# Performance work log

Measured on AMD Instinct MI355X. Metric: run time of the kernel, lower is better.

The kernel has to match this reference:

```python
import jax, jax.numpy as jnp
import numpy as np

B, T, H, L = 64, 2048, 256, 16


def setup_inputs() -> dict:
    key = jax.random.key(0)
    ks = jax.random.split(key, 6)
    x = jax.random.normal(ks[0], (B, T, H), dtype=jnp.float32)
    tags = jax.random.randint(ks[1], (B, T), 0, L).astype(jnp.int32)
    mask = jnp.ones((B, T), dtype=bool)  # torchcrf requires mask[:,0] all on
    W = jax.random.normal(ks[2], (L, H), dtype=jnp.float32) * (1.0 / np.sqrt(H))
    b = jnp.zeros((L,), dtype=jnp.float32)
    # torchcrf initializes transitions ~ U(-0.1, 0.1)
    start_transitions = jax.random.uniform(ks[3], (L,), minval=-0.1, maxval=0.1)
    end_transitions = jax.random.uniform(ks[4], (L,), minval=-0.1, maxval=0.1)
    transitions = jax.random.uniform(ks[5], (L, L), minval=-0.1, maxval=0.1)
    return {"x": x, "W": W, "b": b,
            "start_transitions": start_transitions,
            "end_transitions": end_transitions,
            "transitions": transitions,
            "tags": tags, "mask": mask}


def reference(x, W, b, start_transitions, end_transitions, transitions, tags, mask):
    # Emitter: Linear(hidden_dim -> num_labels)
    emissions = jnp.einsum('bth,lh->btl', x, W) + b  # [B,T,L]
    maskf = mask.astype(emissions.dtype)             # [B,T]

    # ---- numerator: score of the gold tag path (vectorized, no scan) ----
    emit_gold = jnp.take_along_axis(emissions, tags[..., None].astype(jnp.int32), axis=2)[..., 0]  # [B,T]
    first_tags = tags[:, 0]
    score = start_transitions[first_tags] + emit_gold[:, 0]
    trans_gold = transitions[tags[:, :-1], tags[:, 1:]]  # [B,T-1]
    score = score + jnp.sum((trans_gold + emit_gold[:, 1:]) * maskf[:, 1:], axis=1)
    seq_ends = jnp.sum(mask.astype(jnp.int32), axis=1) - 1  # index of last valid step
    last_tags = jnp.take_along_axis(tags, seq_ends[:, None], axis=1)[:, 0]
    score = score + end_transitions[last_tags]

    # ---- denominator: forward algorithm (log partition) via lax.scan over time ----
    em_t = jnp.swapaxes(emissions, 0, 1)  # [T,B,L]
    mask_t = jnp.swapaxes(mask, 0, 1)     # [T,B]
    alpha0 = start_transitions[None, :] + em_t[0]  # [B,L]

    def step(alpha, inp):
        em, m = inp  # em: [B,L], m: [B]
        # logsumexp over previous label: alpha[b,i] + transitions[i,j] + em[b,j]
        nxt = jax.nn.logsumexp(alpha[:, :, None] + transitions[None, :, :] + em[:, None, :], axis=1)
        alpha = jnp.where(m[:, None], nxt, alpha)
        return alpha, None

    alphaT, _ = jax.lax.scan(step, alpha0, (em_t[1:], mask_t[1:]))
    denom = jax.nn.logsumexp(alphaT + end_transitions[None, :], axis=1)  # [B]

    llh = score - denom          # log-likelihood per sequence
    return -jnp.mean(llh)        # reduction='mean', nll = -crf(...)
```

## Files before the change

### kernel.cpp

```cpp
#include <hip/hip_runtime.h>
#include <math.h>


#define Bb 64
#define Tt 2048
#define Hh 256
#define Ll 16
#define CHUNK 32
#define NC (Tt / CHUNK)
#define ROWS 256
#define NCHK (ROWS / CHUNK)

__global__ __launch_bounds__(256) void k_fused(const float* __restrict__ x,
                                               const float* __restrict__ W,
                                               const float* __restrict__ bias,
                                               const float* __restrict__ strans,
                                               const float* __restrict__ etrans,
                                               const float* __restrict__ trans,
                                               const int* __restrict__ tags,
                                               float* __restrict__ em0,
                                               float* __restrict__ Pout,
                                               float* __restrict__ lscale,
                                               float* __restrict__ score) {
  __shared__ float Wl[Ll * Hh];
  __shared__ float tile[ROWS * Ll];
  __shared__ float trl[256];
  __shared__ float etl[256];
  __shared__ float mbuf[ROWS];
  __shared__ float bl[Ll];
  __shared__ float red[256];
  float* ghat = Wl;

  int tid = threadIdx.x;
  int b = blockIdx.x >> 3;
  int t0 = (blockIdx.x & 7) * ROWS;

  for (int idx = tid; idx < Ll * Hh; idx += 256) Wl[idx] = W[idx];
  trl[tid] = trans[tid];
  etl[tid] = expf(trl[tid]);
  if (tid < Ll) bl[tid] = bias[tid];
  __syncthreads();

  {
    int w = tid >> 6, lane = tid & 63, g = lane >> 2, q = lane & 3;
    int rowl = w * 64 + g;
    size_t rowg = (size_t)blockIdx.x * ROWS + rowl;
    const float4* x4 = (const float4*)x;
    float acc[4][16];
#pragma unroll
    for (int r = 0; r < 4; ++r)
#pragma unroll
      for (int l = 0; l < 16; ++l) acc[r][l] = 0.f;
    size_t rb[4];
#pragma unroll
    for (int r = 0; r < 4; ++r) rb[r] = (rowg + (size_t)r * 16) * 64 + q;

#pragma unroll 4
    for (int i = 0; i < 16; ++i) {
      float4 xv0 = x4[rb[0] + i * 4];
      float4 xv1 = x4[rb[1] + i * 4];
      float4 xv2 = x4[rb[2] + i * 4];
      float4 xv3 = x4[rb[3] + i * 4];
      const float* wp = Wl + i * 16 + q * 4;
#pragma unroll
      for (int l = 0; l < 16; ++l) {
        float4 wv = *(const float4*)(wp + l * Hh);
        acc[0][l] = fmaf(xv0.x, wv.x, fmaf(xv0.y, wv.y, fmaf(xv0.z, wv.z, fmaf(xv0.w, wv.w, acc[0][l]))));
        acc[1][l] = fmaf(xv1.x, wv.x, fmaf(xv1.y, wv.y, fmaf(xv1.z, wv.z, fmaf(xv1.w, wv.w, acc[1][l]))));
        acc[2][l] = fmaf(xv2.x, wv.x, fmaf(xv2.y, wv.y, fmaf(xv2.z, wv.z, fmaf(xv2.w, wv.w, acc[2][l]))));
        acc[3][l] = fmaf(xv3.x, wv.x, fmaf(xv3.y, wv.y, fmaf(xv3.z, wv.z, fmaf(xv3.w, wv.w, acc[3][l]))));
      }
    }
    bool qb0 = (q & 1) != 0, qb1 = (q & 2) != 0;
    float4 bq = *(const float4*)(bl + q * 4);
#pragma unroll
    for (int r = 0; r < 4; ++r) {
      float t1[16];
#pragma unroll
      for (int l = 0; l < 16; ++l) t1[l] = __shfl_xor(acc[r][l], 1);
      float r8[8];
#pragma unroll
      for (int k = 0; k < 8; ++k) r8[k] = qb0 ? (acc[r][8 + k] + t1[8 + k]) : (acc[r][k] + t1[k]);
      float t2[8];
#pragma unroll
      for (int k = 0; k < 8; ++k) t2[k] = __shfl_xor(r8[k], 2);
      float r4[4];
#pragma unroll
      for (int k = 0; k < 4; ++k) r4[k] = qb1 ? (r8[4 + k] + t2[4 + k]) : (r8[k] + t2[k]);
      float4 o = make_float4(r4[0] + bq.x, r4[1] + bq.y, r4[2] + bq.z, r4[3] + bq.w);
      *(float4*)(tile + (rowl + r * 16) * 16 + q * 4) = o;
      if (t0 == 0 && r == 0 && tid < 4)
        *(float4*)(em0 + b * 16 + q * 4) = o;
    }
  }
  __syncthreads();

  {
    int gt = blockIdx.x * ROWS + tid;
    int tag = tags[gt];
    float s;
    if ((gt & (Tt - 1)) == 0) {
      s = strans[tag] + tile[tid * 16 + tag];
    } else {
      int pv = tags[gt - 1];
      s = trl[pv * 16 + tag] + tile[tid * 16 + tag];
    }
    if ((gt & (Tt - 1)) == (Tt - 1)) s += etrans[tag];
    red[tid] = s;
    __syncthreads();
    for (int st = 128; st > 0; st >>= 1) {
      if (tid < st) red[tid] += red[tid + st];
      __syncthreads();
    }
    if (tid == 0) atomicAdd(score + b, red[0]);
  }

  {
    const float4* tp = (const float4*)(tile + tid * 16);
    float4 a0 = tp[0], a1 = tp[1], a2 = tp[2], a3 = tp[3];
    float m = fmaxf(fmaxf(fmaxf(fmaxf(a0.x, a0.y), fmaxf(a0.z, a0.w)),
                          fmaxf(fmaxf(a1.x, a1.y), fmaxf(a1.z, a1.w))),
                    fmaxf(fmaxf(fmaxf(a2.x, a2.y), fmaxf(a2.z, a2.w)),
                          fmaxf(fmaxf(a3.x, a3.y), fmaxf(a3.z, a3.w))));
    float4* gp = (float4*)(ghat + tid * 16);
    gp[0] = make_float4(expf(a0.x - m), expf(a0.y - m), expf(a0.z - m), expf(a0.w - m));
    gp[1] = make_float4(expf(a1.x - m), expf(a1.y - m), expf(a1.z - m), expf(a1.w - m));
    gp[2] = make_float4(expf(a2.x - m), expf(a2.y - m), expf(a2.z - m), expf(a2.w - m));
    gp[3] = make_float4(expf(a3.x - m), expf(a3.y - m), expf(a3.z - m), expf(a3.w - m));
    mbuf[tid] = m;
  }
  __syncthreads();

  {
    int w = tid >> 6, lane = tid & 63;
    int i = lane >> 2, jg = lane & 3;
    int srcb = lane & ~3;
    float4 e[16];
#pragma unroll
    for (int k = 0; k < 16; ++k) e[k] = *(const float4*)(etl + k * 16 + jg * 4);

    for (int cc = 0; cc < 2; ++cc) {
      int ci = w + cc * 4;
      int gc = (blockIdx.x & 7) * NCHK + ci;
      int sbeg = (gc == 0) ? 1 : 0;
      float off = 0.f;
      for (int s = sbeg; s < CHUNK; ++s) off += mbuf[ci * CHUNK + s];
      float4 p = make_float4(i == jg * 4 + 0 ? 1.f : 0.f, i == jg * 4 + 1 ? 1.f : 0.f,
                             i == jg * 4 + 2 ? 1.f : 0.f, i == jg * 4 + 3 ? 1.f : 0.f);
      for (int s = sbeg; s < CHUNK; ++s) {
        float4 pm0, pm1, pm2, pm3;
        pm0.x = __shfl(p.x, srcb + 0); pm0.y = __shfl(p.y, srcb + 0);
        pm0.z = __shfl(p.z, srcb + 0); pm0.w = __shfl(p.w, srcb + 0);
        pm1.x = __shfl(p.x, srcb + 1); pm1.y = __shfl(p.y, srcb + 1);
        pm1.z = __shfl(p.z, srcb + 1); pm1.w = __shfl(p.w, srcb + 1);
        pm2.x = __shfl(p.x, srcb + 2); pm2.y = __shfl(p.y, srcb + 2);
        pm2.z = __shfl(p.z, srcb + 2); pm2.w = __shfl(p.w, srcb + 2);
        pm3.x = __shfl(p.x, srcb + 3); pm3.y = __shfl(p.y, srcb + 3);
        pm3.z = __shfl(p.z, srcb + 3); pm3.w = __shfl(p.w, srcb + 3);
        float4 acc = make_float4(0.f, 0.f, 0.f, 0.f);
#define K4ACC(pmv, kb)                                                                \
        acc.x = fmaf(pmv.x, e[kb + 0].x, acc.x); acc.y = fmaf(pmv.x, e[kb + 0].y, acc.y); \
        acc.z = fmaf(pmv.x, e[kb + 0].z, acc.z); acc.w = fmaf(pmv.x, e[kb + 0].w, acc.w); \
        acc.x = fmaf(pmv.y, e[kb + 1].x, acc.x); acc.y = fmaf(pmv.y, e[kb + 1].y, acc.y); \
        acc.z = fmaf(pmv.y, e[kb + 1].z, acc.z); acc.w = fmaf(pmv.y, e[kb + 1].w, acc.w); \
        acc.x = fmaf(pmv.z, e[kb + 2].x, acc.x); acc.y = fmaf(pmv.z, e[kb + 2].y, acc.y); \
        acc.z = fmaf(pmv.z, e[kb + 2].z, acc.z); acc.w = fmaf(pmv.z, e[kb + 2].w, acc.w); \
        acc.x = fmaf(pmv.w, e[kb + 3].x, acc.x); acc.y = fmaf(pmv.w, e[kb + 3].y, acc.y); \
        acc.z = fmaf(pmv.w, e[kb + 3].z, acc.z); acc.w = fmaf(pmv.w, e[kb + 3].w, acc.w);
        K4ACC(pm0, 0) K4ACC(pm1, 4) K4ACC(pm2, 8) K4ACC(pm3, 12)
#undef K4ACC
        float4 g4 = *(const float4*)(ghat + (ci * CHUNK + s) * 16 + jg * 4);
        p.x = acc.x * g4.x; p.y = acc.y * g4.y; p.z = acc.z * g4.z; p.w = acc.w * g4.w;
        if (((s & 7) == 7) || (s == CHUNK - 1)) {
          float mx = fmaxf(fmaxf(p.x, p.y), fmaxf(p.z, p.w));
#pragma unroll
          for (int msk = 1; msk < 64; msk <<= 1) mx = fmaxf(mx, __shfl_xor(mx, msk));
          float inv = __builtin_amdgcn_rcpf(mx);
          p.x *= inv; p.y *= inv; p.z *= inv; p.w *= inv;
          off += logf(mx);
        }
      }
      ((float4*)(Pout + ((size_t)(b * NC + gc)) * 256))[lane] = p;
      if (lane == 0) lscale[b * NC + gc] = off;
    }
  }
}

__global__ __launch_bounds__(64) void k_combine(const float* __restrict__ em0,
                                                const float* __restrict__ P,
                                                const float* __restrict__ lscale,
                                                const float* __restrict__ strans,
                                                const float* __restrict__ etrans,
                                                float* __restrict__ denom) {
  int b = blockIdx.x, lane = threadIdx.x;
  __shared__ float Pl[NC * 256];
  const float4* src = (const float4*)(P + (size_t)b * NC * 256);
  float4* dst = (float4*)Pl;
  for (int idx = lane; idx < NC * 64; idx += 64) dst[idx] = src[idx];
  float ls = lscale[b * NC + lane];
#pragma unroll
  for (int m = 1; m < 64; m <<= 1) ls += __shfl_xor(ls, m);

  int j = lane & 15, ig = lane >> 4;
  float a = strans[j] + em0[b * 16 + j];
  float m0 = a;
#pragma unroll
  for (int m = 1; m < 16; m <<= 1) m0 = fmaxf(m0, __shfl_xor(m0, m));
  float v = expf(a - m0);
  float o = m0 + ls;
  __syncthreads();

  for (int cc = 0; cc < NC; ++cc) {
    const float* Pc = Pl + cc * 256;
    float part = 0.f;
#pragma unroll
    for (int r = 0; r < 4; ++r) {
      int srcl = (ig << 4) + ig * 4 + r;
      float vr = __shfl(v, srcl);
      part = fmaf(vr, Pc[(ig * 4 + r) * 16 + j], part);
    }
    part += __shfl_xor(part, 16);
    part += __shfl_xor(part, 32);
    if ((cc & 3) == 3) {
      float mx = part;
#pragma unroll
      for (int m = 1; m < 16; m <<= 1) mx = fmaxf(mx, __shfl_xor(mx, m));
      o += logf(mx);
      v = part * __builtin_amdgcn_rcpf(mx);
    } else {
      v = part;
    }
  }
  float sj = v * expf(etrans[j]);
#pragma unroll
  for (int m = 1; m < 16; m <<= 1) sj += __shfl_xor(sj, m);
  if (lane == 0) denom[b] = o + logf(sj);
}

__global__ __launch_bounds__(64) void k_final(const float* __restrict__ score,
                                              const float* __restrict__ denom,
                                              float* __restrict__ out) {
  int lane = threadIdx.x;
  float llh = score[lane] - denom[lane];
#pragma unroll
  for (int m = 1; m < 64; m <<= 1) llh += __shfl_xor(llh, m);
  if (lane == 0) out[0] = -llh * (1.0f / 64.0f);
}

extern "C" void kernel_launch(void* const* d_in, const int* in_sizes, int n_in,
                              void* d_out, int out_size, void* d_ws, size_t ws_size,
                              hipStream_t stream) {
  const float* x = (const float*)d_in[0];
  const float* W = (const float*)d_in[1];
  const float* bias = (const float*)d_in[2];
  const float* strans = (const float*)d_in[3];
  const float* etrans = (const float*)d_in[4];
  const float* trans = (const float*)d_in[5];
  const int* tags = (const int*)d_in[6];

  float* ws = (float*)d_ws;
  float* em0 = ws;
  float* P = em0 + Bb * 16;
  float* lscale = P + (size_t)Bb * NC * 256;
  float* score = lscale + Bb * NC;
  float* denom = score + Bb;
  float* out = (float*)d_out;

  hipMemsetAsync(score, 0, Bb * sizeof(float), stream);
  hipLaunchKernelGGL(k_fused, dim3(Bb * Tt / ROWS), dim3(256), 0, stream,
                     x, W, bias, strans, etrans, trans, tags, em0, P, lscale, score);
  hipLaunchKernelGGL(k_combine, dim3(Bb), dim3(64), 0, stream, em0, P, lscale, strans, etrans, denom);
  hipLaunchKernelGGL(k_final, dim3(1), dim3(64), 0, stream, score, denom, out);
}
```

Before: 274.0 us.

## Halve rows per block, pad LDS tile, and use wave-shuffle score reduction

Each block now covers 128 timesteps instead of 256, which doubles the grid to 1024 blocks. Each wave then runs one chunk of the sequential scan instead of two, and holds two rows of matmul accumulators instead of four, which lowers register pressure. The emission tile gets a padded stride of 20 floats to reduce LDS bank conflicts, and the gold-score reduction becomes a wave shuffle reduction with per-wave atomics in place of the shared-memory tree. The risk is more blocks each reloading W and the transition tables, plus four times as many atomics on the score.

```diff
diff --git a/kernel.cpp b/kernel.cpp
--- a/kernel.cpp
+++ b/kernel.cpp
@@ -8,8 +8,9 @@
 #define Ll 16
 #define CHUNK 32
 #define NC (Tt / CHUNK)
-#define ROWS 256
+#define ROWS 128
 #define NCHK (ROWS / CHUNK)
+#define TSTR 20
 
 __global__ __launch_bounds__(256) void k_fused(const float* __restrict__ x,
                                                const float* __restrict__ W,
@@ -23,17 +24,17 @@
                                                float* __restrict__ lscale,
                                                float* __restrict__ score) {
   __shared__ float Wl[Ll * Hh];
-  __shared__ float tile[ROWS * Ll];
+  __shared__ float tile[ROWS * TSTR];
   __shared__ float trl[256];
   __shared__ float etl[256];
   __shared__ float mbuf[ROWS];
   __shared__ float bl[Ll];
-  __shared__ float red[256];
   float* ghat = Wl;
 
   int tid = threadIdx.x;
-  int b = blockIdx.x >> 3;
-  int t0 = (blockIdx.x & 7) * ROWS;
+  int b = blockIdx.x >> 4;
+  int blk = blockIdx.x & 15;
+  int t0 = blk * ROWS;
 
   for (int idx = tid; idx < Ll * Hh; idx += 256) Wl[idx] = W[idx];
   trl[tid] = trans[tid];
@@ -41,40 +42,37 @@
   if (tid < Ll) bl[tid] = bias[tid];
   __syncthreads();
 
+  int w = tid >> 6, lane = tid & 63;
+
   {
-    int w = tid >> 6, lane = tid & 63, g = lane >> 2, q = lane & 3;
-    int rowl = w * 64 + g;
+    int g = lane >> 2, q = lane & 3;
+    int rowl = w * 32 + g;
     size_t rowg = (size_t)blockIdx.x * ROWS + rowl;
     const float4* x4 = (const float4*)x;
-    float acc[4][16];
-#pragma unroll
-    for (int r = 0; r < 4; ++r)
+    float acc[2][16];
+#pragma unroll
+    for (int r = 0; r < 2; ++r)
 #pragma unroll
       for (int l = 0; l < 16; ++l) acc[r][l] = 0.f;
-    size_t rb[4];
-#pragma unroll
-    for (int r = 0; r < 4; ++r) rb[r] = (rowg + (size_t)r * 16) * 64 + q;
+    size_t rb0 = rowg * 64 + q;
+    size_t rb1 = (rowg + 16) * 64 + q;
 
 #pragma unroll 4
     for (int i = 0; i < 16; ++i) {
-      float4 xv0 = x4[rb[0] + i * 4];
-      float4 xv1 = x4[rb[1] + i * 4];
-      float4 xv2 = x4[rb[2] + i * 4];
-      float4 xv3 = x4[rb[3] + i * 4];
+      float4 xv0 = x4[rb0 + i * 4];
+      float4 xv1 = x4[rb1 + i * 4];
       const float* wp = Wl + i * 16 + q * 4;
 #pragma unroll
       for (int l = 0; l < 16; ++l) {
         float4 wv = *(const float4*)(wp + l * Hh);
         acc[0][l] = fmaf(xv0.x, wv.x, fmaf(xv0.y, wv.y, fmaf(xv0.z, wv.z, fmaf(xv0.w, wv.w, acc[0][l]))));
         acc[1][l] = fmaf(xv1.x, wv.x, fmaf(xv1.y, wv.y, fmaf(xv1.z, wv.z, fmaf(xv1.w, wv.w, acc[1][l]))));
-        acc[2][l] = fmaf(xv2.x, wv.x, fmaf(xv2.y, wv.y, fmaf(xv2.z, wv.z, fmaf(xv2.w, wv.w, acc[2][l]))));
-        acc[3][l] = fmaf(xv3.x, wv.x, fmaf(xv3.y, wv.y, fmaf(xv3.z, wv.z, fmaf(xv3.w, wv.w, acc[3][l]))));
       }
     }
     bool qb0 = (q & 1) != 0, qb1 = (q & 2) != 0;
     float4 bq = *(const float4*)(bl + q * 4);
 #pragma unroll
-    for (int r = 0; r < 4; ++r) {
+    for (int r = 0; r < 2; ++r) {
       float t1[16];
 #pragma unroll
       for (int l = 0; l < 16; ++l) t1[l] = __shfl_xor(acc[r][l], 1);
@@ -88,41 +86,21 @@
 #pragma unroll
       for (int k = 0; k < 4; ++k) r4[k] = qb1 ? (r8[4 + k] + t2[4 + k]) : (r8[k] + t2[k]);
       float4 o = make_float4(r4[0] + bq.x, r4[1] + bq.y, r4[2] + bq.z, r4[3] + bq.w);
-      *(float4*)(tile + (rowl + r * 16) * 16 + q * 4) = o;
+      *(float4*)(tile + (rowl + r * 16) * TSTR + q * 4) = o;
       if (t0 == 0 && r == 0 && tid < 4)
         *(float4*)(em0 + b * 16 + q * 4) = o;
     }
   }
   __syncthreads();
 
-  {
-    int gt = blockIdx.x * ROWS + tid;
-    int tag = tags[gt];
-    float s;
-    if ((gt & (Tt - 1)) == 0) {
-      s = strans[tag] + tile[tid * 16 + tag];
-    } else {
-      int pv = tags[gt - 1];
-      s = trl[pv * 16 + tag] + tile[tid * 16 + tag];
-    }
-    if ((gt & (Tt - 1)) == (Tt - 1)) s += etrans[tag];
-    red[tid] = s;
-    __syncthreads();
-    for (int st = 128; st > 0; st >>= 1) {
-      if (tid < st) red[tid] += red[tid + st];
-      __syncthreads();
-    }
-    if (tid == 0) atomicAdd(score + b, red[0]);
-  }
-
-  {
-    const float4* tp = (const float4*)(tile + tid * 16);
+  if (tid < ROWS) {
+    const float4* tp = (const float4*)(tile + tid * TSTR);
     float4 a0 = tp[0], a1 = tp[1], a2 = tp[2], a3 = tp[3];
     float m = fmaxf(fmaxf(fmaxf(fmaxf(a0.x, a0.y), fmaxf(a0.z, a0.w)),
                           fmaxf(fmaxf(a1.x, a1.y), fmaxf(a1.z, a1.w))),
                     fmaxf(fmaxf(fmaxf(a2.x, a2.y), fmaxf(a2.z, a2.w)),
                           fmaxf(fmaxf(a3.x, a3.y), fmaxf(a3.z, a3.w))));
-    float4* gp = (float4*)(ghat + tid * 16);
+    float4* gp = (float4*)(ghat + tid * TSTR);
     gp[0] = make_float4(expf(a0.x - m), expf(a0.y - m), expf(a0.z - m), expf(a0.w - m));
     gp[1] = make_float4(expf(a1.x - m), expf(a1.y - m), expf(a1.z - m), expf(a1.w - m));
     gp[2] = make_float4(expf(a2.x - m), expf(a2.y - m), expf(a2.z - m), expf(a2.w - m));
@@ -132,57 +110,74 @@
   __syncthreads();
 
   {
-    int w = tid >> 6, lane = tid & 63;
+    float s = 0.f;
+    if (lane < 32) {
+      int rl = w * 32 + lane;
+      int t = t0 + rl;
+      int gt = b * Tt + t;
+      int tag = tags[gt];
+      if (t == 0) {
+        s = strans[tag] + tile[rl * TSTR + tag];
+      } else {
+        int pv = tags[gt - 1];
+        s = trl[pv * 16 + tag] + tile[rl * TSTR + tag];
+      }
+      if (t == Tt - 1) s += etrans[tag];
+    }
+#pragma unroll
+    for (int m = 1; m < 64; m <<= 1) s += __shfl_xor(s, m);
+    if (lane == 0) atomicAdd(score + b, s);
+  }
+
+  {
     int i = lane >> 2, jg = lane & 3;
     int srcb = lane & ~3;
     float4 e[16];
 #pragma unroll
     for (int k = 0; k < 16; ++k) e[k] = *(const float4*)(etl + k * 16 + jg * 4);
 
-    for (int cc = 0; cc < 2; ++cc) {
-      int ci = w + cc * 4;
-      int gc = (blockIdx.x & 7) * NCHK + ci;
-      int sbeg = (gc == 0) ? 1 : 0;
-      float off = 0.f;
-      for (int s = sbeg; s < CHUNK; ++s) off += mbuf[ci * CHUNK + s];
-      float4 p = make_float4(i == jg * 4 + 0 ? 1.f : 0.f, i == jg * 4 + 1 ? 1.f : 0.f,
-                             i == jg * 4 + 2 ? 1.f : 0.f, i == jg * 4 + 3 ? 1.f : 0.f);
-      for (int s = sbeg; s < CHUNK; ++s) {
-        float4 pm0, pm1, pm2, pm3;
-        pm0.x = __shfl(p.x, srcb + 0); pm0.y = __shfl(p.y, srcb + 0);
-        pm0.z = __shfl(p.z, srcb + 0); pm0.w = __shfl(p.w, srcb + 0);
-        pm1.x = __shfl(p.x, srcb + 1); pm1.y = __shfl(p.y, srcb + 1);
-        pm1.z = __shfl(p.z, srcb + 1); pm1.w = __shfl(p.w, srcb + 1);
-        pm2.x = __shfl(p.x, srcb + 2); pm2.y = __shfl(p.y, srcb + 2);
-        pm2.z = __shfl(p.z, srcb + 2); pm2.w = __shfl(p.w, srcb + 2);
-        pm3.x = __shfl(p.x, srcb + 3); pm3.y = __shfl(p.y, srcb + 3);
-        pm3.z = __shfl(p.z, srcb + 3); pm3.w = __shfl(p.w, srcb + 3);
-        float4 acc = make_float4(0.f, 0.f, 0.f, 0.f);
+    int ci = w;
+    int gc = blk * NCHK + ci;
+    int sbeg = (gc == 0) ? 1 : 0;
+    float off = 0.f;
+    for (int s = sbeg; s < CHUNK; ++s) off += mbuf[ci * CHUNK + s];
+    float4 p = make_float4(i == jg * 4 + 0 ? 1.f : 0.f, i == jg * 4 + 1 ? 1.f : 0.f,
+                           i == jg * 4 + 2 ? 1.f : 0.f, i == jg * 4 + 3 ? 1.f : 0.f);
+    for (int s = sbeg; s < CHUNK; ++s) {
+      float4 pm0, pm1, pm2, pm3;
+      pm0.x = __shfl(p.x, srcb + 0); pm0.y = __shfl(p.y, srcb + 0);
+      pm0.z = __shfl(p.z, srcb + 0); pm0.w = __shfl(p.w, srcb + 0);
+      pm1.x = __shfl(p.x, srcb + 1); pm1.y = __shfl(p.y, srcb + 1);
+      pm1.z = __shfl(p.z, srcb + 1); pm1.w = __shfl(p.w, srcb + 1);
+      pm2.x = __shfl(p.x, srcb + 2); pm2.y = __shfl(p.y, srcb + 2);
+      pm2.z = __shfl(p.z, srcb + 2); pm2.w = __shfl(p.w, srcb + 2);
+      pm3.x = __shfl(p.x, srcb + 3); pm3.y = __shfl(p.y, srcb + 3);
+      pm3.z = __shfl(p.z, srcb + 3); pm3.w = __shfl(p.w, srcb + 3);
+      float4 acc = make_float4(0.f, 0.f, 0.f, 0.f);
 #define K4ACC(pmv, kb)                                                                \
-        acc.x = fmaf(pmv.x, e[kb + 0].x, acc.x); acc.y = fmaf(pmv.x, e[kb + 0].y, acc.y); \
-        acc.z = fmaf(pmv.x, e[kb + 0].z, acc.z); acc.w = fmaf(pmv.x, e[kb + 0].w, acc.w); \
-        acc.x = fmaf(pmv.y, e[kb + 1].x, acc.x); acc.y = fmaf(pmv.y, e[kb + 1].y, acc.y); \
-        acc.z = fmaf(pmv.y, e[kb + 1].z, acc.z); acc.w = fmaf(pmv.y, e[kb + 1].w, acc.w); \
-        acc.x = fmaf(pmv.z, e[kb + 2].x, acc.x); acc.y = fmaf(pmv.z, e[kb + 2].y, acc.y); \
-        acc.z = fmaf(pmv.z, e[kb + 2].z, acc.z); acc.w = fmaf(pmv.z, e[kb + 2].w, acc.w); \
-        acc.x = fmaf(pmv.w, e[kb + 3].x, acc.x); acc.y = fmaf(pmv.w, e[kb + 3].y, acc.y); \
-        acc.z = fmaf(pmv.w, e[kb + 3].z, acc.z); acc.w = fmaf(pmv.w, e[kb + 3].w, acc.w);
-        K4ACC(pm0, 0) K4ACC(pm1, 4) K4ACC(pm2, 8) K4ACC(pm3, 12)
+      acc.x = fmaf(pmv.x, e[kb + 0].x, acc.x); acc.y = fmaf(pmv.x, e[kb + 0].y, acc.y); \
+      acc.z = fmaf(pmv.x, e[kb + 0].z, acc.z); acc.w = fmaf(pmv.x, e[kb + 0].w, acc.w); \
+      acc.x = fmaf(pmv.y, e[kb + 1].x, acc.x); acc.y = fmaf(pmv.y, e[kb + 1].y, acc.y); \
+      acc.z = fmaf(pmv.y, e[kb + 1].z, acc.z); acc.w = fmaf(pmv.y, e[kb + 1].w, acc.w); \
+      acc.x = fmaf(pmv.z, e[kb + 2].x, acc.x); acc.y = fmaf(pmv.z, e[kb + 2].y, acc.y); \
+      acc.z = fmaf(pmv.z, e[kb + 2].z, acc.z); acc.w = fmaf(pmv.z, e[kb + 2].w, acc.w); \
+      acc.x = fmaf(pmv.w, e[kb + 3].x, acc.x); acc.y = fmaf(pmv.w, e[kb + 3].y, acc.y); \
+      acc.z = fmaf(pmv.w, e[kb + 3].z, acc.z); acc.w = fmaf(pmv.w, e[kb + 3].w, acc.w);
+      K4ACC(pm0, 0) K4ACC(pm1, 4) K4ACC(pm2, 8) K4ACC(pm3, 12)
 #undef K4ACC
-        float4 g4 = *(const float4*)(ghat + (ci * CHUNK + s) * 16 + jg * 4);
-        p.x = acc.x * g4.x; p.y = acc.y * g4.y; p.z = acc.z * g4.z; p.w = acc.w * g4.w;
-        if (((s & 7) == 7) || (s == CHUNK - 1)) {
-          float mx = fmaxf(fmaxf(p.x, p.y), fmaxf(p.z, p.w));
-#pragma unroll
-          for (int msk = 1; msk < 64; msk <<= 1) mx = fmaxf(mx, __shfl_xor(mx, msk));
-          float inv = __builtin_amdgcn_rcpf(mx);
-          p.x *= inv; p.y *= inv; p.z *= inv; p.w *= inv;
-          off += logf(mx);
-        }
+      float4 g4 = *(const float4*)(ghat + (ci * CHUNK + s) * TSTR + jg * 4);
+      p.x = acc.x * g4.x; p.y = acc.y * g4.y; p.z = acc.z * g4.z; p.w = acc.w * g4.w;
+      if (((s & 7) == 7) || (s == CHUNK - 1)) {
+        float mx = fmaxf(fmaxf(p.x, p.y), fmaxf(p.z, p.w));
+#pragma unroll
+        for (int msk = 1; msk < 64; msk <<= 1) mx = fmaxf(mx, __shfl_xor(mx, msk));
+        float inv = __builtin_amdgcn_rcpf(mx);
+        p.x *= inv; p.y *= inv; p.z *= inv; p.w *= inv;
+        off += logf(mx);
       }
-      ((float4*)(Pout + ((size_t)(b * NC + gc)) * 256))[lane] = p;
-      if (lane == 0) lscale[b * NC + gc] = off;
-    }
+    }
+    ((float4*)(Pout + ((size_t)(b * NC + gc)) * 256))[lane] = p;
+    if (lane == 0) lscale[b * NC + gc] = off;
   }
 }
 
```

Result: slower. 283.0 us (+3.3%).
